# Optimization experiments

Measured on AMD Instinct MI355X. Metric: run time of the kernel, lower is better.

The kernel has to match this reference:

```python
import jax, jax.numpy as jnp
import numpy as np

B, S, D, F, H, E = 2, 1024, 1024, 4096, 16, 8
EPS = 1e-5


def _layernorm(x, w, b):
    m = jnp.mean(x, -1, keepdims=True)
    v = jnp.var(x, -1, keepdims=True)
    return (x - m) * jax.lax.rsqrt(v + EPS) * w + b


def _rope(x):
    # rotary embedding applied over full embed dim (split-half convention)
    b, s, d = x.shape
    half = d // 2
    inv = 1.0 / (10000.0 ** (jnp.arange(half, dtype=jnp.float32) / half))
    ang = jnp.arange(s, dtype=jnp.float32)[:, None] * inv[None, :]  # [S, half]
    cos, sin = jnp.cos(ang), jnp.sin(ang)
    x1, x2 = x[..., :half], x[..., half:]
    return jnp.concatenate([x1 * cos - x2 * sin, x1 * sin + x2 * cos], -1)


def setup_inputs() -> dict:
    key = jax.random.key(0)
    ks = jax.random.split(key, 9)
    sc = 0.02
    return {
        "x": jax.random.normal(ks[0], (B, S, D), jnp.float32),
        "ln1_w": jnp.ones((D,), jnp.float32),
        "ln1_b": jnp.zeros((D,), jnp.float32),
        "ln2_w": jnp.ones((D,), jnp.float32),
        "ln2_b": jnp.zeros((D,), jnp.float32),
        "w_qkv": jax.random.normal(ks[1], (3 * D, D), jnp.float32) * sc,
        "b_qkv": jnp.zeros((3 * D,), jnp.float32),
        "w_out": jax.random.normal(ks[2], (D, D), jnp.float32) * sc,
        "b_out": jnp.zeros((D,), jnp.float32),
        "w_router": jax.random.normal(ks[3], (D, E), jnp.float32) * sc,
        "wi": jax.random.normal(ks[4], (E, D, F), jnp.float32) * sc,  # per-expert wi (no bias)
        "wo": jax.random.normal(ks[5], (E, F // 2, D), jnp.float32) * sc,  # swiglu halves ffn dim
    }


def reference(x, ln1_w, ln1_b, ln2_w, ln2_b, w_qkv, b_qkv, w_out, b_out, w_router, wi, wo):
    # ---- pre-norm self-attention block ----
    residual = x
    h = _layernorm(x, ln1_w, ln1_b)
    h = _rope(h)
    qkv = h @ w_qkv.T + b_qkv  # [B,S,3D]
    q, k, v = jnp.split(qkv, 3, axis=-1)
    hd = D // H
    to_heads = lambda t: t.reshape(B, S, H, hd).transpose(0, 2, 1, 3)
    q, k, v = to_heads(q), to_heads(k), to_heads(v)
    scale = 1.0 / np.sqrt(hd).astype(np.float32)
    att = jax.nn.softmax(jnp.einsum('bhqd,bhkd->bhqk', q, k) * scale, axis=-1)
    o = jnp.einsum('bhqk,bhkd->bhqd', att, v).transpose(0, 2, 1, 3).reshape(B, S, D)
    o = o @ w_out.T + b_out
    x = residual + o  # attn dropout is identity at eval

    # ---- pre-norm sparse MoE FFN block ----
    residual = x
    h = _layernorm(x, ln2_w, ln2_b)
    # top-1 router in float32
    logits = h.astype(jnp.float32) @ w_router  # [B,S,E]
    probs = jax.nn.softmax(logits, axis=-1)
    mask = jax.nn.one_hot(jnp.argmax(probs, -1), E, dtype=h.dtype)  # expert_mask
    gate = probs.astype(h.dtype) * mask  # router_probs * expert_mask, [B,S,E]
    # dense all-expert compute, masked combine (same math as gather/scatter loop)
    hid = jnp.einsum('bsd,edf->bsef', h, wi)  # [B,S,E,F]
    a, g = jnp.split(hid, 2, axis=-1)
    act = jax.nn.silu(a) * g  # SwiGLU, [B,S,E,F/2]
    y = jnp.einsum('bsef,efd,bse->bsd', act, wo, gate)
    x = residual + y
    return x, logits
```

## Files before the change

kernel.cpp:

```cpp
#include <hip/hip_runtime.h>
#include <hip/hip_bf16.h>
#include <math.h>

#define BB 2
#define SS 1024
#define DD 1024
#define FF 4096
#define HH 16
#define EE 8
#define MM (BB*SS)
#define MAX_TILES 24

typedef __attribute__((ext_vector_type(8))) short bf16x8;
typedef __attribute__((ext_vector_type(8))) short s16x8;
typedef __attribute__((ext_vector_type(4))) float f32x4;

#define OFF_WIT  ((size_t)0)
#define OFF_WOT  ((size_t)67108864)
#define OFF_WQH  ((size_t)100663296)
#define OFF_WQL  ((size_t)106954752)
#define OFF_WOH  ((size_t)113246208)
#define OFF_WOL  ((size_t)115343360)
#define OFF_H1H  ((size_t)117440512)
#define OFF_H1L  ((size_t)121634816)
#define OFF_QKV  ((size_t)125829120)
#define OFF_OH   ((size_t)150994944)
#define OFF_OL   ((size_t)155189248)
#define OFF_X2   ((size_t)159383552)
#define OFF_H2B  ((size_t)167772160)
#define OFF_ACT  ((size_t)171966464)
#define OFF_GATE ((size_t)180879360)
#define OFF_EID  ((size_t)180887552)
#define OFF_PERM ((size_t)180895744)
#define OFF_CNT  ((size_t)180903936)
#define OFF_FILL ((size_t)180903968)
#define OFF_NT   ((size_t)180904000)
#define OFF_TE   ((size_t)180904192)
#define OFF_TS   ((size_t)180904320)
#define OFF_TR   ((size_t)180904448)
#define OFF_KSH  OFF_WQH
#define OFF_KSL  (OFF_WQH + 4194304)
#define OFF_VTH  OFF_H1H
#define OFF_VTL  OFF_H1L

__device__ __forceinline__ void gload16(const void* g, void* l) {
    __builtin_amdgcn_global_load_lds(
        (const __attribute__((address_space(1))) unsigned int*)g,
        (__attribute__((address_space(3))) unsigned int*)l, 16, 0, 0);
}

__device__ __forceinline__ short bfh(float v) {
    __hip_bfloat16 h = __float2bfloat16(v);
    return *(short*)&h;
}
__device__ __forceinline__ float bf2f(short s) {
    __hip_bfloat16 h = *(__hip_bfloat16*)&s;
    return __bfloat162float(h);
}

__device__ __forceinline__ void split_write(float v, __hip_bfloat16* hp, __hip_bfloat16* lp, size_t idx) {
    __hip_bfloat16 h = __float2bfloat16(v);
    hp[idx] = h;
    lp[idx] = __float2bfloat16(v - __bfloat162float(h));
}

__device__ __forceinline__ void tcvt64_body(const float* __restrict__ in, __hip_bfloat16* __restrict__ out,
                                            int R, int C, int r0, int c0, float* tile ) {
    int t = threadIdx.x;
    {
        int ri = t >> 2, cj = (t & 3) * 16;
        const float* ip = &in[(size_t)(r0 + ri) * C + c0 + cj];
#pragma unroll
        for (int k = 0; k < 4; ++k) {
            float4 v = *(const float4*)(ip + k * 4);
            tile[ri * 65 + cj + k * 4 + 0] = v.x;
            tile[ri * 65 + cj + k * 4 + 1] = v.y;
            tile[ri * 65 + cj + k * 4 + 2] = v.z;
            tile[ri * 65 + cj + k * 4 + 3] = v.w;
        }
    }
    __syncthreads();
    {
        int co = t >> 2, rj = (t & 3) * 16;
        bf16x8 v8a, v8b;
#pragma unroll
        for (int q = 0; q < 8; ++q) v8a[q] = bfh(tile[(rj + q) * 65 + co]);
#pragma unroll
        for (int q = 0; q < 8; ++q) v8b[q] = bfh(tile[(rj + 8 + q) * 65 + co]);
        __hip_bfloat16* op = &out[(size_t)(c0 + co) * R + r0 + rj];
        *(bf16x8*)op = v8a;
        *(bf16x8*)(op + 8) = v8b;
    }
}

__global__ void k_phase0(const float* __restrict__ x, const float* __restrict__ ln1w,
                         const float* __restrict__ ln1b,
                         __hip_bfloat16* __restrict__ h1H, __hip_bfloat16* __restrict__ h1L,
                         const float* __restrict__ w_qkv, __hip_bfloat16* __restrict__ wqH,
                         __hip_bfloat16* __restrict__ wqL,
                         const float* __restrict__ w_out, __hip_bfloat16* __restrict__ woH,
                         __hip_bfloat16* __restrict__ woL,
                         const float* __restrict__ wi, __hip_bfloat16* __restrict__ wiT,
                         const float* __restrict__ wo, __hip_bfloat16* __restrict__ woT) {
    __shared__ __align__(16) float smem[64 * 65];
    int bid = blockIdx.x, t = threadIdx.x;
    if (bid < 2048) {
        int m = bid, s = m & (SS - 1);
        float* row = smem;
        float* red = smem + 1024;
        const float* xp = x + (size_t)m * DD;
        float sum = 0.f, sumsq = 0.f;
#pragma unroll
        for (int l = 0; l < 4; ++l) {
            int i = t + l * 256;
            float v = xp[i];
            row[i] = v;
            sum += v; sumsq += v * v;
        }
#pragma unroll
        for (int off = 32; off; off >>= 1) {
            sum   += __shfl_xor(sum, off);
            sumsq += __shfl_xor(sumsq, off);
        }
        int wid = t >> 6, lane = t & 63;
        if (lane == 0) { red[wid] = sum; red[4 + wid] = sumsq; }
        __syncthreads();
        sum   = red[0] + red[1] + red[2] + red[3];
        sumsq = red[4] + red[5] + red[6] + red[7];
        float mean = sum * (1.f / DD);
        float var  = sumsq * (1.f / DD) - mean * mean;
        float rstd = rsqrtf(var + 1e-5f);
        size_t base = (size_t)m * DD;
        const float kln = logf(10000.f) / 512.f;
#pragma unroll
        for (int l = 0; l < 2; ++l) {
            int i = t + l * 256;
            float n1 = (row[i]       - mean) * rstd * ln1w[i]       + ln1b[i];
            float n2 = (row[i + 512] - mean) * rstd * ln1w[i + 512] + ln1b[i + 512];
            float inv = expf(-(float)i * kln);
            float ang = (float)s * inv;
            float c = cosf(ang), sn = sinf(ang);
            split_write(n1 * c - n2 * sn,  h1H, h1L, base + i);
            split_write(n1 * sn + n2 * c, h1H, h1L, base + i + 512);
        }
    } else if (bid < 6144) {
        int i = (bid - 2048) * 256 + t;
        const float* in; __hip_bfloat16 *hi, *lo; int idx;
        if (i < 786432) { in = w_qkv; hi = wqH; lo = wqL; idx = i; }
        else            { idx = i - 786432; in = w_out; hi = woH; lo = woL; }
        float4 v = ((const float4*)in)[idx];
        split_write(v.x, hi, lo, (size_t)idx * 4 + 0);
        split_write(v.y, hi, lo, (size_t)idx * 4 + 1);
        split_write(v.z, hi, lo, (size_t)idx * 4 + 2);
        split_write(v.w, hi, lo, (size_t)idx * 4 + 3);
    } else if (bid < 14336) {
        int j = bid - 6144;
        int e = j >> 10, rem = j & 1023;
        int ry = rem >> 6, cx = rem & 63;
        tcvt64_body(wi + (size_t)e * DD * FF, (__hip_bfloat16*)wiT + (size_t)e * DD * FF,
                    1024, 4096, ry * 64, cx * 64, smem);
    } else {
        int j = bid - 14336;
        int e = j >> 9, rem = j & 511;
        int ry = rem >> 4, cx = rem & 15;
        tcvt64_body(wo + (size_t)e * 2048 * 1024, (__hip_bfloat16*)woT + (size_t)e * 2048 * 1024,
                    2048, 1024, ry * 64, cx * 64, smem);
    }
}

template<int MODE>
__global__ void k_mfma_split(const __hip_bfloat16* __restrict__ Ah, const __hip_bfloat16* __restrict__ Al,
                             const __hip_bfloat16* __restrict__ Bh, const __hip_bfloat16* __restrict__ Bl,
                             const float* __restrict__ bias, const float* __restrict__ addsrc,
                             float* __restrict__ Cf, int M, int N, int K, int* __restrict__ zero17) {
    __shared__ __align__(16) short AsH[128 * 32];
    __shared__ __align__(16) short AsL[128 * 32];
    __shared__ __align__(16) short BsH[128 * 32];
    __shared__ __align__(16) short BsL[128 * 32];
    int m0 = blockIdx.y * 128, n0 = blockIdx.x * 128;
    const int t = threadIdx.x;
    if (MODE == 1 && blockIdx.x == 0 && blockIdx.y == 0 && t < 17) zero17[t] = 0;
    const int w = t >> 6, lane = t & 63;
    const int wr = w >> 1, wc = w & 1;
    const int sid = w * 64 + lane;

    f32x4 acc[4][4] = {};

    for (int k0 = 0; k0 < K; k0 += 32) {
#pragma unroll
        for (int j = 0; j < 2; ++j) {
            int id = j * 256 + sid;
            int rrow = id >> 2, sl = id & 3;
            int slog = sl ^ ((rrow >> 1) & 3);
            size_t lbase = (size_t)(j * 256 + w * 64) * 8;
            size_t gaoff = (size_t)(m0 + rrow) * K + k0 + slog * 8;
            gload16(Ah + gaoff, &AsH[lbase]);
            gload16(Al + gaoff, &AsL[lbase]);
            size_t gboff = (size_t)(n0 + rrow) * K + k0 + slog * 8;
            gload16(Bh + gboff, &BsH[lbase]);
            gload16(Bl + gboff, &BsL[lbase]);
        }
        __syncthreads();
        bf16x8 ah[4], al[4], bh[4], bl[4];
#pragma unroll
        for (int i = 0; i < 4; ++i) {
            int ra = wr * 64 + i * 16 + (lane & 15);
            int pa = (lane >> 4) ^ ((ra >> 1) & 3);
            ah[i] = *(const bf16x8*)&AsH[ra * 32 + pa * 8];
            al[i] = *(const bf16x8*)&AsL[ra * 32 + pa * 8];
            int rb = wc * 64 + i * 16 + (lane & 15);
            int pb = (lane >> 4) ^ ((rb >> 1) & 3);
            bh[i] = *(const bf16x8*)&BsH[rb * 32 + pb * 8];
            bl[i] = *(const bf16x8*)&BsL[rb * 32 + pb * 8];
        }
#pragma unroll
        for (int i = 0; i < 4; ++i)
#pragma unroll
            for (int n = 0; n < 4; ++n) {
                acc[i][n] = __builtin_amdgcn_mfma_f32_16x16x32_bf16(ah[i], bh[n], acc[i][n], 0, 0, 0);
                acc[i][n] = __builtin_amdgcn_mfma_f32_16x16x32_bf16(ah[i], bl[n], acc[i][n], 0, 0, 0);
                acc[i][n] = __builtin_amdgcn_mfma_f32_16x16x32_bf16(al[i], bh[n], acc[i][n], 0, 0, 0);
            }
        __syncthreads();
    }

    int cn = n0 + wc * 64 + (lane & 15);
#pragma unroll
    for (int i = 0; i < 4; ++i) {
#pragma unroll
        for (int n = 0; n < 4; ++n) {
            int col = cn + n * 16;
#pragma unroll
            for (int q = 0; q < 4; ++q) {
                int r = wr * 64 + i * 16 + (lane >> 4) * 4 + q;
                float v = acc[i][n][q] + bias[col];
                if (MODE == 1) v += addsrc[(size_t)(m0 + r) * N + col];
                Cf[(size_t)(m0 + r) * N + col] = v;
            }
        }
    }
}

__global__ void k_moe_up(const __hip_bfloat16* __restrict__ A,
                         const __hip_bfloat16* __restrict__ Bt,
                         __hip_bfloat16* __restrict__ act,
                         const int* __restrict__ perm,
                         const int* __restrict__ te, const int* __restrict__ ts,
                         const int* __restrict__ tr, const int* __restrict__ ntl) {
    __shared__ __align__(16) short As[128 * 32];
    __shared__ __align__(16) short Bs[128 * 32];
    __shared__ int permS[128];
    int tile = blockIdx.y;
    if (tile >= *ntl) return;
    int e = te[tile], rs = ts[tile], rows = tr[tile];
    if (threadIdx.x < 128) {
        int r = threadIdx.x;
        permS[r] = (r < rows) ? perm[rs + r] : 0;
    }
    __syncthreads();
    int c0 = blockIdx.x * 64;
    const int t = threadIdx.x;
    const int w = t >> 6, lane = t & 63;
    const int wr = w >> 1, wc = w & 1;
    const int sid = w * 64 + lane;
    const int g = lane >> 4, r16 = lane & 15;

    const __hip_bfloat16* Bp = Bt + (size_t)e * FF * DD;

    f32x4 acc[4][4] = {};

    for (int k0 = 0; k0 < DD; k0 += 32) {
#pragma unroll
        for (int j = 0; j < 2; ++j) {
            int id = j * 256 + sid;
            int rrow = id >> 2, sl = id & 3;
            int slog = sl ^ ((rrow >> 1) & 3);
            size_t lbase = (size_t)(j * 256 + w * 64) * 8;
            gload16(A + (size_t)permS[rrow] * DD + k0 + slog * 8, &As[lbase]);
            int q = rrow >> 4, rr = rrow & 15;
            int wrow = c0 + (q >> 2) * 32 + ((q & 3) >> 1) * 16 + rr + (q & 1) * 2048;
            gload16(Bp + (size_t)wrow * DD + k0 + slog * 8, &Bs[lbase]);
        }
        __syncthreads();
        bf16x8 af[4], bfr[4];
#pragma unroll
        for (int i = 0; i < 4; ++i) {
            int ra = wr * 64 + i * 16 + r16;
            int pa = g ^ ((ra >> 1) & 3);
            af[i] = *(const bf16x8*)&As[ra * 32 + pa * 8];
            int rb = wc * 64 + i * 16 + r16;
            int pb = g ^ ((rb >> 1) & 3);
            bfr[i] = *(const bf16x8*)&Bs[rb * 32 + pb * 8];
        }
#pragma unroll
        for (int i = 0; i < 4; ++i)
#pragma unroll
            for (int n = 0; n < 4; ++n)
                acc[i][n] = __builtin_amdgcn_mfma_f32_16x16x32_bf16(af[i], bfr[n], acc[i][n], 0, 0, 0);
        __syncthreads();
    }

#pragma unroll
    for (int i = 0; i < 4; ++i) {
#pragma unroll
        for (int p2 = 0; p2 < 2; ++p2) {
            int col = c0 + wc * 32 + p2 * 16 + r16;
#pragma unroll
            for (int q = 0; q < 4; ++q) {
                int r = wr * 64 + i * 16 + g * 4 + q;
                if (r < rows) {
                    float a  = acc[i][2 * p2][q];
                    float gv = acc[i][2 * p2 + 1][q];
                    act[(size_t)(rs + r) * 2048 + col] =
                        __float2bfloat16((a / (1.f + expf(-a))) * gv);
                }
            }
        }
    }
}

__global__ void k_moe_dn(const __hip_bfloat16* __restrict__ A,
                         const __hip_bfloat16* __restrict__ Bt,
                         const float* __restrict__ addsrc, float* __restrict__ Cf,
                         const int* __restrict__ perm,
                         const int* __restrict__ te, const int* __restrict__ ts,
                         const int* __restrict__ tr, const int* __restrict__ ntl,
                         const float* __restrict__ gate) {
    __shared__ __align__(16) short As[128 * 32];
    __shared__ __align__(16) short Bs[128 * 32];
    __shared__ int permS[128];
    int tile = blockIdx.y;
    if (tile >= *ntl) return;
    int e = te[tile], rs = ts[tile], rows = tr[tile];
    if (threadIdx.x < 128) {
        int r = threadIdx.x;
        permS[r] = (r < rows) ? perm[rs + r] : 0;
    }
    __syncthreads();
    int n0 = blockIdx.x * 128;
    const int t = threadIdx.x;
    const int w = t >> 6, lane = t & 63;
    const int wr = w >> 1, wc = w & 1;
    const int sid = w * 64 + lane;
    const int K = FF / 2;

    const __hip_bfloat16* Bp = Bt + (size_t)e * DD * (FF / 2);

    f32x4 acc[4][4] = {};

    for (int k0 = 0; k0 < K; k0 += 32) {
#pragma unroll
        for (int j = 0; j < 2; ++j) {
            int id = j * 256 + sid;
            int rrow = id >> 2, sl = id & 3;
            int slog = sl ^ ((rrow >> 1) & 3);
            size_t lbase = (size_t)(j * 256 + w * 64) * 8;
            gload16(A + (size_t)(rs + rrow) * K + k0 + slog * 8, &As[lbase]);
            gload16(Bp + (size_t)(n0 + rrow) * K + k0 + slog * 8, &Bs[lbase]);
        }
        __syncthreads();
        bf16x8 af[4], bfr[4];
#pragma unroll
        for (int i = 0; i < 4; ++i) {
            int ra = wr * 64 + i * 16 + (lane & 15);
            int pa = (lane >> 4) ^ ((ra >> 1) & 3);
            af[i] = *(const bf16x8*)&As[ra * 32 + pa * 8];
            int rb = wc * 64 + i * 16 + (lane & 15);
            int pb = (lane >> 4) ^ ((rb >> 1) & 3);
            bfr[i] = *(const bf16x8*)&Bs[rb * 32 + pb * 8];
        }
#pragma unroll
        for (int i = 0; i < 4; ++i)
#pragma unroll
            for (int n = 0; n < 4; ++n)
                acc[i][n] = __builtin_amdgcn_mfma_f32_16x16x32_bf16(af[i], bfr[n], acc[i][n], 0, 0, 0);
        __syncthreads();
    }

    int cn = n0 + wc * 64 + (lane & 15);
#pragma unroll
    for (int i = 0; i < 4; ++i) {
#pragma unroll
        for (int n = 0; n < 4; ++n) {
            int col = cn + n * 16;
#pragma unroll
            for (int q = 0; q < 4; ++q) {
                int r = wr * 64 + i * 16 + (lane >> 4) * 4 + q;
                if (r >= rows) continue;
                int tok = permS[r];
                Cf[(size_t)tok * DD + col] = addsrc[(size_t)tok * DD + col] + gate[tok] * acc[i][n][q];
            }
        }
    }
}

__global__ void k_prep(const float* __restrict__ qkv, short* __restrict__ KH, short* __restrict__ KL,
                       short* __restrict__ VH, short* __restrict__ VL) {
    __shared__ float tile[64][65];
    int b = blockIdx.z, h = blockIdx.y, s0 = blockIdx.x * 64;
    int t = threadIdx.x;
    int row = t >> 2, c0 = (t & 3) * 16;
    const float* kp = qkv + (size_t)(b * SS + s0 + row) * 3072 + 1024 + h * 64 + c0;
    const float* vp = kp + 1024;
    {
        size_t krow = ((size_t)(b * HH + h) * SS + s0 + row) * 64;
        int key = (s0 + row) & 7;
#pragma unroll
        for (int g2 = 0; g2 < 2; ++g2) {
            s16x8 hv, lv;
#pragma unroll
            for (int j = 0; j < 8; ++j) {
                float v = kp[g2 * 8 + j];
                short hh = bfh(v);
                hv[j] = hh; lv[j] = bfh(v - bf2f(hh));
            }
            int p = ((c0 >> 3) + g2) ^ key;
            *(s16x8*)&KH[krow + p * 8] = hv;
            *(s16x8*)&KL[krow + p * 8] = lv;
        }
    }
#pragma unroll
    for (int j = 0; j < 16; ++j) tile[row][c0 + j] = vp[j];
    __syncthreads();
    {
        int d = t >> 2, sc = (t & 3) * 16;
        size_t vrow = ((size_t)(b * HH + h) * 64 + d) * SS + s0;
        int key = d & 7;
#pragma unroll
        for (int g2 = 0; g2 < 2; ++g2) {
            s16x8 hv, lv;
#pragma unroll
            for (int j = 0; j < 8; ++j) {
                float v = tile[sc + g2 * 8 + j][d];
                short hh = bfh(v);
                hv[j] = hh; lv[j] = bfh(v - bf2f(hh));
            }
            int p = ((sc >> 3) + g2) ^ key;
            *(s16x8*)&VH[vrow + p * 8] = hv;
            *(s16x8*)&VL[vrow + p * 8] = lv;
        }
    }
}

#define LDP 72
__global__ __launch_bounds__(512, 1)
void k_attn_mfma(const float* __restrict__ qkv,
                 const short* __restrict__ KH, const short* __restrict__ KL,
                 const short* __restrict__ VH, const short* __restrict__ VL,
                 __hip_bfloat16* __restrict__ ohi, __hip_bfloat16* __restrict__ olo) {
    __shared__ __align__(16) short Ks[2][64 * 64], Kl2[2][64 * 64], Vs[2][64 * 64], Vl2[2][64 * 64];
    __shared__ __align__(16) short PhS[8][16 * LDP], PlS[8][16 * LDP];
    int id = blockIdx.x;
    int xcd = id & 7, slot = id >> 3;
    int bh = xcd * 4 + (slot >> 3);
    int q0 = (slot & 7) * 128;
    int b = bh >> 4, h = bh & 15;
    int t = threadIdx.x;
    int w = t >> 6, lane = t & 63;
    int g = lane >> 4, r16 = lane & 15;
    int srow = t >> 3, sslot = t & 7;

    const size_t kbase = ((size_t)bh * SS) * 64;
    const size_t vbase = ((size_t)bh * 64) * SS;

    bf16x8 qfh[2], qfl[2];
    {
        const float* qp = qkv + (size_t)(b * SS + q0 + w * 16 + r16) * 3072 + h * 64;
#pragma unroll
        for (int ks = 0; ks < 2; ++ks) {
            float vv[8];
            *(float4*)&vv[0] = *(const float4*)(qp + ks * 32 + g * 8);
            *(float4*)&vv[4] = *(const float4*)(qp + ks * 32 + g * 8 + 4);
#pragma unroll
            for (int j = 0; j < 8; ++j) {
                float sv = vv[j] * 0.125f;
                short hh = bfh(sv);
                qfh[ks][j] = hh;
                qfl[ks][j] = bfh(sv - bf2f(hh));
            }
        }
    }

    float mrun[4], lrun[4];
    f32x4 oacc[4] = {};
#pragma unroll
    for (int q = 0; q < 4; ++q) { mrun[q] = -1e30f; lrun[q] = 0.f; }

    gload16(KH + kbase + (size_t)srow * 64 + sslot * 8, &Ks[0][w * 512]);
    gload16(KL + kbase + (size_t)srow * 64 + sslot * 8, &Kl2[0][w * 512]);
    gload16(VH + vbase + (size_t)srow * SS + sslot * 8, &Vs[0][w * 512]);
    gload16(VL + vbase + (size_t)srow * SS + sslot * 8, &Vl2[0][w * 512]);
    __syncthreads();

    int cur = 0;
    for (int k0 = 0; k0 < SS; k0 += 64) {
        if (k0 + 64 < SS) {
            int kn = k0 + 64;
            gload16(KH + kbase + (size_t)(kn + srow) * 64 + sslot * 8, &Ks[cur ^ 1][w * 512]);
            gload16(KL + kbase + (size_t)(kn + srow) * 64 + sslot * 8, &Kl2[cur ^ 1][w * 512]);
            gload16(VH + vbase + (size_t)srow * SS + kn + sslot * 8,   &Vs[cur ^ 1][w * 512]);
            gload16(VL + vbase + (size_t)srow * SS + kn + sslot * 8,   &Vl2[cur ^ 1][w * 512]);
        }

        f32x4 accs[4] = {};
#pragma unroll
        for (int ks = 0; ks < 2; ++ks) {
            bf16x8 kfh[4], kfl[4];
#pragma unroll
            for (int n = 0; n < 4; ++n) {
                int rb = n * 16 + r16;
                int p = (ks * 4 + g) ^ (r16 & 7);
                kfh[n] = *(const bf16x8*)&Ks[cur][rb * 64 + p * 8];
                kfl[n] = *(const bf16x8*)&Kl2[cur][rb * 64 + p * 8];
            }
            __builtin_amdgcn_s_setprio(1);
#pragma unroll
            for (int n = 0; n < 4; ++n) {
                accs[n] = __builtin_amdgcn_mfma_f32_16x16x32_bf16(qfh[ks], kfh[n], accs[n], 0, 0, 0);
                accs[n] = __builtin_amdgcn_mfma_f32_16x16x32_bf16(qfh[ks], kfl[n], accs[n], 0, 0, 0);
                accs[n] = __builtin_amdgcn_mfma_f32_16x16x32_bf16(qfl[ks], kfh[n], accs[n], 0, 0, 0);
            }
            __builtin_amdgcn_s_setprio(0);
        }

        float mn[4], corr[4], psum[4];
#pragma unroll
        for (int q = 0; q < 4; ++q) {
            float m = fmaxf(fmaxf(accs[0][q], accs[1][q]), fmaxf(accs[2][q], accs[3][q]));
            m = fmaxf(m, __shfl_xor(m, 1));
            m = fmaxf(m, __shfl_xor(m, 2));
            m = fmaxf(m, __shfl_xor(m, 4));
            m = fmaxf(m, __shfl_xor(m, 8));
            mn[q] = fmaxf(mrun[q], m);
            corr[q] = expf(mrun[q] - mn[q]);
            mrun[q] = mn[q];
            psum[q] = 0.f;
        }
#pragma unroll
        for (int n = 0; n < 4; ++n)
#pragma unroll
            for (int q = 0; q < 4; ++q) {
                float p = expf(accs[n][q] - mn[q]);
                psum[q] += p;
                short ph = bfh(p);
                PhS[w][(g * 4 + q) * LDP + n * 16 + r16] = ph;
                PlS[w][(g * 4 + q) * LDP + n * 16 + r16] = bfh(p - bf2f(ph));
            }
#pragma unroll
        for (int q = 0; q < 4; ++q) {
            psum[q] += __shfl_xor(psum[q], 1);
            psum[q] += __shfl_xor(psum[q], 2);
            psum[q] += __shfl_xor(psum[q], 4);
            psum[q] += __shfl_xor(psum[q], 8);
            lrun[q] = lrun[q] * corr[q] + psum[q];
#pragma unroll
            for (int n = 0; n < 4; ++n) oacc[n][q] *= corr[q];
        }

#pragma unroll
        for (int ks = 0; ks < 2; ++ks) {
            bf16x8 vfh[4], vfl[4];
#pragma unroll
            for (int n = 0; n < 4; ++n) {
                int rb = n * 16 + r16;
                int p = (ks * 4 + g) ^ (r16 & 7);
                vfh[n] = *(const bf16x8*)&Vs[cur][rb * 64 + p * 8];
                vfl[n] = *(const bf16x8*)&Vl2[cur][rb * 64 + p * 8];
            }
            bf16x8 pfh = *(const bf16x8*)&PhS[w][r16 * LDP + ks * 32 + g * 8];
            bf16x8 pfl = *(const bf16x8*)&PlS[w][r16 * LDP + ks * 32 + g * 8];
            __builtin_amdgcn_s_setprio(1);
#pragma unroll
            for (int n = 0; n < 4; ++n) {
                oacc[n] = __builtin_amdgcn_mfma_f32_16x16x32_bf16(pfh, vfh[n], oacc[n], 0, 0, 0);
                oacc[n] = __builtin_amdgcn_mfma_f32_16x16x32_bf16(pfh, vfl[n], oacc[n], 0, 0, 0);
                oacc[n] = __builtin_amdgcn_mfma_f32_16x16x32_bf16(pfl, vfh[n], oacc[n], 0, 0, 0);
            }
            __builtin_amdgcn_s_setprio(0);
        }
        __syncthreads();
        cur ^= 1;
    }

    float invl[4];
#pragma unroll
    for (int q = 0; q < 4; ++q) invl[q] = 1.f / lrun[q];
#pragma unroll
    for (int n = 0; n < 4; ++n) {
        int col = h * 64 + n * 16 + r16;
#pragma unroll
        for (int q = 0; q < 4; ++q) {
            int rowg = b * SS + q0 + w * 16 + g * 4 + q;
            split_write(oacc[n][q] * invl[q], ohi, olo, (size_t)rowg * DD + col);
        }
    }
}

__global__ void k_ln2_router(const float* __restrict__ x2, const float* __restrict__ w,
                             const float* __restrict__ b, const float* __restrict__ wr,
                             __hip_bfloat16* __restrict__ h2b, float* __restrict__ logits,
                             float* __restrict__ gate, int* __restrict__ eid,
                             int* __restrict__ counts) {
    int m = blockIdx.x, t = threadIdx.x;
    __shared__ float red[8];
    __shared__ float racc[4][8];
    const float* xp = x2 + (size_t)m * DD;
    float v[4];
    float sum = 0.f, sumsq = 0.f;
#pragma unroll
    for (int l = 0; l < 4; ++l) {
        v[l] = xp[t + l * 256];
        sum += v[l]; sumsq += v[l] * v[l];
    }
#pragma unroll
    for (int off = 32; off; off >>= 1) {
        sum   += __shfl_xor(sum, off);
        sumsq += __shfl_xor(sumsq, off);
    }
    int wid = t >> 6, lane = t & 63;
    if (lane == 0) { red[wid] = sum; red[4 + wid] = sumsq; }
    __syncthreads();
    sum   = red[0] + red[1] + red[2] + red[3];
    sumsq = red[4] + red[5] + red[6] + red[7];
    float mean = sum * (1.f / DD);
    float var  = sumsq * (1.f / DD) - mean * mean;
    float rstd = rsqrtf(var + 1e-5f);
    float acc[EE] = {};
#pragma unroll
    for (int l = 0; l < 4; ++l) {
        int i = t + l * 256;
        float hv = (v[l] - mean) * rstd * w[i] + b[i];
        h2b[(size_t)m * DD + i] = __float2bfloat16(hv);
        const float* wp = wr + (size_t)i * EE;
#pragma unroll
        for (int n = 0; n < EE; ++n) acc[n] += hv * wp[n];
    }
#pragma unroll
    for (int off = 32; off; off >>= 1)
#pragma unroll
        for (int n = 0; n < EE; ++n) acc[n] += __shfl_xor(acc[n], off);
    if (lane == 0)
#pragma unroll
        for (int n = 0; n < EE; ++n) racc[wid][n] = acc[n];
    __syncthreads();
    if (t == 0) {
        float lg[EE];
#pragma unroll
        for (int n = 0; n < EE; ++n) lg[n] = racc[0][n] + racc[1][n] + racc[2][n] + racc[3][n];
        float mx = lg[0]; int best = 0;
#pragma unroll
        for (int n = 1; n < EE; ++n) if (lg[n] > mx) { mx = lg[n]; best = n; }
        float den = 0.f;
#pragma unroll
        for (int n = 0; n < EE; ++n) den += expf(lg[n] - mx);
        gate[m] = 1.f / den;
        eid[m] = best;
        atomicAdd(&counts[best], 1);
#pragma unroll
        for (int n = 0; n < EE; ++n) logits[(size_t)m * EE + n] = lg[n];
    }
}

__global__ void k_offscatter(const int* __restrict__ counts,
                             int* __restrict__ te, int* __restrict__ ts, int* __restrict__ tr,
                             int* __restrict__ ntl, const int* __restrict__ eid,
                             int* __restrict__ fill, int* __restrict__ perm) {
    __shared__ int soffs[EE];
    int t = threadIdx.x;
    if (t == 0) {
        int off = 0, nt = 0;
        for (int e = 0; e < EE; ++e) {
            soffs[e] = off;
            int c = counts[e];
            for (int t0 = 0; t0 < c; t0 += 128) {
                te[nt] = e; ts[nt] = off + t0; tr[nt] = (c - t0 < 128) ? (c - t0) : 128; ++nt;
            }
            off += c;
        }
        *ntl = nt;
    }
    __syncthreads();
#pragma unroll
    for (int tok = t; tok < MM; tok += 1024) {
        int e = eid[tok];
        int pos = soffs[e] + atomicAdd(&fill[e], 1);
        perm[pos] = tok;
    }
}

extern "C" void kernel_launch(void* const* d_in, const int* in_sizes, int n_in,
                              void* d_out, int out_size, void* d_ws, size_t ws_size,
                              hipStream_t stream) {
    const float* x     = (const float*)d_in[0];
    const float* ln1w  = (const float*)d_in[1];
    const float* ln1b  = (const float*)d_in[2];
    const float* ln2w  = (const float*)d_in[3];
    const float* ln2b  = (const float*)d_in[4];
    const float* w_qkv = (const float*)d_in[5];
    const float* b_qkv = (const float*)d_in[6];
    const float* w_out = (const float*)d_in[7];
    const float* b_out = (const float*)d_in[8];
    const float* w_rtr = (const float*)d_in[9];
    const float* wi    = (const float*)d_in[10];
    const float* wo    = (const float*)d_in[11];
    float* out = (float*)d_out;

    char* wsb = (char*)d_ws;
    __hip_bfloat16* wiT  = (__hip_bfloat16*)(wsb + OFF_WIT);
    __hip_bfloat16* woT  = (__hip_bfloat16*)(wsb + OFF_WOT);
    __hip_bfloat16* wqH  = (__hip_bfloat16*)(wsb + OFF_WQH);
    __hip_bfloat16* wqL  = (__hip_bfloat16*)(wsb + OFF_WQL);
    __hip_bfloat16* woH  = (__hip_bfloat16*)(wsb + OFF_WOH);
    __hip_bfloat16* woL  = (__hip_bfloat16*)(wsb + OFF_WOL);
    __hip_bfloat16* h1H  = (__hip_bfloat16*)(wsb + OFF_H1H);
    __hip_bfloat16* h1L  = (__hip_bfloat16*)(wsb + OFF_H1L);
    float*          qkvF = (float*)(wsb + OFF_QKV);
    __hip_bfloat16* oH   = (__hip_bfloat16*)(wsb + OFF_OH);
    __hip_bfloat16* oL   = (__hip_bfloat16*)(wsb + OFF_OL);
    float*          x2F  = (float*)(wsb + OFF_X2);
    __hip_bfloat16* h2B  = (__hip_bfloat16*)(wsb + OFF_H2B);
    __hip_bfloat16* actB = (__hip_bfloat16*)(wsb + OFF_ACT);
    short* KSH = (short*)(wsb + OFF_KSH);
    short* KSL = (short*)(wsb + OFF_KSL);
    short* VTH = (short*)(wsb + OFF_VTH);
    short* VTL = (short*)(wsb + OFF_VTL);
    float* gate = (float*)(wsb + OFF_GATE);
    int* eid    = (int*)(wsb + OFF_EID);
    int* perm   = (int*)(wsb + OFF_PERM);
    int* counts = (int*)(wsb + OFF_CNT);
    int* fill   = (int*)(wsb + OFF_FILL);
    int* ntl    = (int*)(wsb + OFF_NT);
    int* te     = (int*)(wsb + OFF_TE);
    int* tsx    = (int*)(wsb + OFF_TS);
    int* trx    = (int*)(wsb + OFF_TR);

    k_phase0<<<18432, 256, 0, stream>>>(x, ln1w, ln1b, h1H, h1L,
                                        w_qkv, wqH, wqL, w_out, woH, woL,
                                        wi, wiT, wo, woT);
    k_mfma_split<0><<<dim3(3072 / 128, MM / 128), 256, 0, stream>>>(
        h1H, h1L, wqH, wqL, b_qkv, nullptr, qkvF, MM, 3072, DD, nullptr);
    k_prep<<<dim3(SS / 64, HH, BB), 256, 0, stream>>>(qkvF, KSH, KSL, VTH, VTL);
    k_attn_mfma<<<256, 512, 0, stream>>>(qkvF, KSH, KSL, VTH, VTL, oH, oL);
    k_mfma_split<1><<<dim3(DD / 128, MM / 128), 256, 0, stream>>>(
        oH, oL, woH, woL, b_out, x, x2F, MM, DD, DD, counts);
    k_ln2_router<<<MM, 256, 0, stream>>>(x2F, ln2w, ln2b, w_rtr, h2B,
                                         out + (size_t)MM * DD, gate, eid, counts);
    k_offscatter<<<1, 1024, 0, stream>>>(counts, te, tsx, trx, ntl, eid, fill, perm);
    k_moe_up<<<dim3(2048 / 64, MAX_TILES), 256, 0, stream>>>(
        h2B, wiT, actB, perm, te, tsx, trx, ntl);
    k_moe_dn<<<dim3(DD / 128, MAX_TILES), 256, 0, stream>>>(
        actB, woT, x2F, out, perm, te, tsx, trx, ntl, gate);
}
```

Before: 370.5 us.

## Overlap MoE weight transposes with QKV GEMM in a single merged launch

Moves the wi/wo transpose-to-bf16 blocks and the w_out split conversion out of phase0 and into one launch with the QKV projection GEMM. The GEMM blocks come first, so the memory-bound conversion blocks can fill idle compute units while the GEMM tiles run. Phase0 now handles only LN1+RoPE and the w_qkv split, which shrinks it and lets the GEMM start sooner. The cost is that all blocks of the merged kernel are sized for the larger 32KB shared-memory footprint, which can lower occupancy for the conversion blocks, and the GEMM's 384 blocks now compete with about 13k copy blocks for scheduling.

```diff
diff --git a/kernel.cpp b/kernel.cpp
--- a/kernel.cpp
+++ b/kernel.cpp
@@ -97,12 +97,8 @@
                          const float* __restrict__ ln1b,
                          __hip_bfloat16* __restrict__ h1H, __hip_bfloat16* __restrict__ h1L,
                          const float* __restrict__ w_qkv, __hip_bfloat16* __restrict__ wqH,
-                         __hip_bfloat16* __restrict__ wqL,
-                         const float* __restrict__ w_out, __hip_bfloat16* __restrict__ woH,
-                         __hip_bfloat16* __restrict__ woL,
-                         const float* __restrict__ wi, __hip_bfloat16* __restrict__ wiT,
-                         const float* __restrict__ wo, __hip_bfloat16* __restrict__ woT) {
-    __shared__ __align__(16) float smem[64 * 65];
+                         __hip_bfloat16* __restrict__ wqL) {
+    __shared__ __align__(16) float smem[1032];
     int bid = blockIdx.x, t = threadIdx.x;
     if (bid < 2048) {
         int m = bid, s = m & (SS - 1);
@@ -143,43 +139,123 @@
             split_write(n1 * c - n2 * sn,  h1H, h1L, base + i);
             split_write(n1 * sn + n2 * c, h1H, h1L, base + i + 512);
         }
-    } else if (bid < 6144) {
-        int i = (bid - 2048) * 256 + t;
-        const float* in; __hip_bfloat16 *hi, *lo; int idx;
-        if (i < 786432) { in = w_qkv; hi = wqH; lo = wqL; idx = i; }
-        else            { idx = i - 786432; in = w_out; hi = woH; lo = woL; }
-        float4 v = ((const float4*)in)[idx];
-        split_write(v.x, hi, lo, (size_t)idx * 4 + 0);
-        split_write(v.y, hi, lo, (size_t)idx * 4 + 1);
-        split_write(v.z, hi, lo, (size_t)idx * 4 + 2);
-        split_write(v.w, hi, lo, (size_t)idx * 4 + 3);
-    } else if (bid < 14336) {
-        int j = bid - 6144;
+    } else {
+        int idx = (bid - 2048) * 256 + t;
+        float4 v = ((const float4*)w_qkv)[idx];
+        split_write(v.x, wqH, wqL, (size_t)idx * 4 + 0);
+        split_write(v.y, wqH, wqL, (size_t)idx * 4 + 1);
+        split_write(v.z, wqH, wqL, (size_t)idx * 4 + 2);
+        split_write(v.w, wqH, wqL, (size_t)idx * 4 + 3);
+    }
+}
+
+__global__ void k_qkv_mega(const __hip_bfloat16* __restrict__ Ah, const __hip_bfloat16* __restrict__ Al,
+                           const __hip_bfloat16* __restrict__ Bh, const __hip_bfloat16* __restrict__ Bl,
+                           const float* __restrict__ bias, float* __restrict__ Cf,
+                           const float* __restrict__ wi, __hip_bfloat16* __restrict__ wiT,
+                           const float* __restrict__ wo, __hip_bfloat16* __restrict__ woT,
+                           const float* __restrict__ w_out, __hip_bfloat16* __restrict__ woH,
+                           __hip_bfloat16* __restrict__ woL) {
+    __shared__ __align__(16) char smem[32768];
+    int bid = blockIdx.x;
+    const int t = threadIdx.x;
+    if (bid < 384) {
+        const int N = 3072, K = DD;
+        short* AsH = (short*)smem;
+        short* AsL = (short*)(smem + 8192);
+        short* BsH = (short*)(smem + 16384);
+        short* BsL = (short*)(smem + 24576);
+        int n0 = (bid % 24) * 128, m0 = (bid / 24) * 128;
+        const int w = t >> 6, lane = t & 63;
+        const int wr = w >> 1, wc = w & 1;
+        const int sid = w * 64 + lane;
+
+        f32x4 acc[4][4] = {};
+
+        for (int k0 = 0; k0 < K; k0 += 32) {
+#pragma unroll
+            for (int j = 0; j < 2; ++j) {
+                int id = j * 256 + sid;
+                int rrow = id >> 2, sl = id & 3;
+                int slog = sl ^ ((rrow >> 1) & 3);
+                size_t lbase = (size_t)(j * 256 + w * 64) * 8;
+                size_t gaoff = (size_t)(m0 + rrow) * K + k0 + slog * 8;
+                gload16(Ah + gaoff, &AsH[lbase]);
+                gload16(Al + gaoff, &AsL[lbase]);
+                size_t gboff = (size_t)(n0 + rrow) * K + k0 + slog * 8;
+                gload16(Bh + gboff, &BsH[lbase]);
+                gload16(Bl + gboff, &BsL[lbase]);
+            }
+            __syncthreads();
+            bf16x8 ah[4], al[4], bh[4], bl[4];
+#pragma unroll
+            for (int i = 0; i < 4; ++i) {
+                int ra = wr * 64 + i * 16 + (lane & 15);
+                int pa = (lane >> 4) ^ ((ra >> 1) & 3);
+                ah[i] = *(const bf16x8*)&AsH[ra * 32 + pa * 8];
+                al[i] = *(const bf16x8*)&AsL[ra * 32 + pa * 8];
+                int rb = wc * 64 + i * 16 + (lane & 15);
+                int pb = (lane >> 4) ^ ((rb >> 1) & 3);
+                bh[i] = *(const bf16x8*)&BsH[rb * 32 + pb * 8];
+                bl[i] = *(const bf16x8*)&BsL[rb * 32 + pb * 8];
+            }
+#pragma unroll
+            for (int i = 0; i < 4; ++i)
+#pragma unroll
+                for (int n = 0; n < 4; ++n) {
+                    acc[i][n] = __builtin_amdgcn_mfma_f32_16x16x32_bf16(ah[i], bh[n], acc[i][n], 0, 0, 0);
+                    acc[i][n] = __builtin_amdgcn_mfma_f32_16x16x32_bf16(ah[i], bl[n], acc[i][n], 0, 0, 0);
+                    acc[i][n] = __builtin_amdgcn_mfma_f32_16x16x32_bf16(al[i], bh[n], acc[i][n], 0, 0, 0);
+                }
+            __syncthreads();
+        }
+
+        int cn = n0 + wc * 64 + (lane & 15);
+#pragma unroll
+        for (int i = 0; i < 4; ++i) {
+#pragma unroll
+            for (int n = 0; n < 4; ++n) {
+                int col = cn + n * 16;
+#pragma unroll
+                for (int q = 0; q < 4; ++q) {
+                    int r = wr * 64 + i * 16 + (lane >> 4) * 4 + q;
+                    Cf[(size_t)(m0 + r) * N + col] = acc[i][n][q] + bias[col];
+                }
+            }
+        }
+    } else if (bid < 8576) {
+        int j = bid - 384;
         int e = j >> 10, rem = j & 1023;
         int ry = rem >> 6, cx = rem & 63;
-        tcvt64_body(wi + (size_t)e * DD * FF, (__hip_bfloat16*)wiT + (size_t)e * DD * FF,
-                    1024, 4096, ry * 64, cx * 64, smem);
-    } else {
-        int j = bid - 14336;
+        tcvt64_body(wi + (size_t)e * DD * FF, wiT + (size_t)e * DD * FF,
+                    1024, 4096, ry * 64, cx * 64, (float*)smem);
+    } else if (bid < 12672) {
+        int j = bid - 8576;
         int e = j >> 9, rem = j & 511;
         int ry = rem >> 4, cx = rem & 15;
-        tcvt64_body(wo + (size_t)e * 2048 * 1024, (__hip_bfloat16*)woT + (size_t)e * 2048 * 1024,
-                    2048, 1024, ry * 64, cx * 64, smem);
-    }
-}
-
-template<int MODE>
-__global__ void k_mfma_split(const __hip_bfloat16* __restrict__ Ah, const __hip_bfloat16* __restrict__ Al,
-                             const __hip_bfloat16* __restrict__ Bh, const __hip_bfloat16* __restrict__ Bl,
-                             const float* __restrict__ bias, const float* __restrict__ addsrc,
-                             float* __restrict__ Cf, int M, int N, int K, int* __restrict__ zero17) {
+        tcvt64_body(wo + (size_t)e * 2048 * 1024, woT + (size_t)e * 2048 * 1024,
+                    2048, 1024, ry * 64, cx * 64, (float*)smem);
+    } else {
+        int idx = (bid - 12672) * 256 + t;
+        float4 v = ((const float4*)w_out)[idx];
+        split_write(v.x, woH, woL, (size_t)idx * 4 + 0);
+        split_write(v.y, woH, woL, (size_t)idx * 4 + 1);
+        split_write(v.z, woH, woL, (size_t)idx * 4 + 2);
+        split_write(v.w, woH, woL, (size_t)idx * 4 + 3);
+    }
+}
+
+__global__ void k_mfma_split1(const __hip_bfloat16* __restrict__ Ah, const __hip_bfloat16* __restrict__ Al,
+                              const __hip_bfloat16* __restrict__ Bh, const __hip_bfloat16* __restrict__ Bl,
+                              const float* __restrict__ bias, const float* __restrict__ addsrc,
+                              float* __restrict__ Cf, int M, int N, int K, int* __restrict__ zero17) {
     __shared__ __align__(16) short AsH[128 * 32];
     __shared__ __align__(16) short AsL[128 * 32];
     __shared__ __align__(16) short BsH[128 * 32];
     __shared__ __align__(16) short BsL[128 * 32];
     int m0 = blockIdx.y * 128, n0 = blockIdx.x * 128;
     const int t = threadIdx.x;
-    if (MODE == 1 && blockIdx.x == 0 && blockIdx.y == 0 && t < 17) zero17[t] = 0;
+    if (blockIdx.x == 0 && blockIdx.y == 0 && t < 17) zero17[t] = 0;
     const int w = t >> 6, lane = t & 63;
     const int wr = w >> 1, wc = w & 1;
     const int sid = w * 64 + lane;
@@ -233,9 +309,8 @@
 #pragma unroll
             for (int q = 0; q < 4; ++q) {
                 int r = wr * 64 + i * 16 + (lane >> 4) * 4 + q;
-                float v = acc[i][n][q] + bias[col];
-                if (MODE == 1) v += addsrc[(size_t)(m0 + r) * N + col];
-                Cf[(size_t)(m0 + r) * N + col] = v;
+                Cf[(size_t)(m0 + r) * N + col] =
+                    acc[i][n][q] + bias[col] + addsrc[(size_t)(m0 + r) * N + col];
             }
         }
     }
@@ -734,14 +809,12 @@
     int* tsx    = (int*)(wsb + OFF_TS);
     int* trx    = (int*)(wsb + OFF_TR);
 
-    k_phase0<<<18432, 256, 0, stream>>>(x, ln1w, ln1b, h1H, h1L,
-                                        w_qkv, wqH, wqL, w_out, woH, woL,
-                                        wi, wiT, wo, woT);
-    k_mfma_split<0><<<dim3(3072 / 128, MM / 128), 256, 0, stream>>>(
-        h1H, h1L, wqH, wqL, b_qkv, nullptr, qkvF, MM, 3072, DD, nullptr);
+    k_phase0<<<5120, 256, 0, stream>>>(x, ln1w, ln1b, h1H, h1L, w_qkv, wqH, wqL);
+    k_qkv_mega<<<13696, 256, 0, stream>>>(h1H, h1L, wqH, wqL, b_qkv, qkvF,
+                                          wi, wiT, wo, woT, w_out, woH, woL);
     k_prep<<<dim3(SS / 64, HH, BB), 256, 0, stream>>>(qkvF, KSH, KSL, VTH, VTL);
     k_attn_mfma<<<256, 512, 0, stream>>>(qkvF, KSH, KSL, VTH, VTL, oH, oL);
-    k_mfma_split<1><<<dim3(DD / 128, MM / 128), 256, 0, stream>>>(
+    k_mfma_split1<<<dim3(DD / 128, MM / 128), 256, 0, stream>>>(
         oH, oL, woH, woL, b_out, x, x2F, MM, DD, DD, counts);
     k_ln2_router<<<MM, 256, 0, stream>>>(x2F, ln2w, ln2b, w_rtr, h2B,
                                          out + (size_t)MM * DD, gate, eid, counts);
```

After: 334.9 us. 9.6% less time.
